# Kernel optimization log

Hardware: AMD Instinct MI355X
Metric: run time of the kernel (lower is better)

Reference implementation:

```python
import jax, jax.numpy as jnp
import numpy as np

TOP_K = 8


def setup_inputs() -> dict:
    key = jax.random.key(0)
    ks = jax.random.split(key, 8)
    B, S, H, BD, N, VBD = 4, 2048, 2048, 256, 256, 256
    return {
        "hidden_states": jax.random.normal(ks[0], (B, S, H), jnp.float32),
        "primary_attention_output": jax.random.normal(ks[1], (B, S, H), jnp.float32),
        "q_proj_w": jax.random.normal(ks[2], (BD, H), jnp.float32) / np.sqrt(H),
        "slot_keys": jax.random.normal(ks[3], (N, BD), jnp.float32),
        "slot_values": jax.random.normal(ks[4], (N, H), jnp.float32),
        "reliability": jax.random.uniform(ks[5], (N,), jnp.float32, 1e-3, 1.0),
        "value_down_w": jax.random.normal(ks[6], (VBD, H), jnp.float32) * 0.1 / np.sqrt(H),
        "value_up_w": jax.random.normal(ks[7], (H, VBD), jnp.float32) * 0.1 / np.sqrt(VBD),
    }


def reference(hidden_states, primary_attention_output, q_proj_w, slot_keys,
              slot_values, reliability, value_down_w, value_up_w):
    B, S, H = hidden_states.shape
    BD = q_proj_w.shape[0]
    # query = q_proj(hidden_states): [B,S,BD]
    query = jnp.einsum("bsh,dh->bsd", hidden_states, q_proj_w)
    # gate-chain scoring: query . slot_keys scaled, plus log-reliability mask
    rel_mask = jnp.log(jnp.clip(reliability, 1e-10))            # [N]
    scores = jnp.einsum("bsd,nd->bsn", query, slot_keys) / jnp.sqrt(
        jnp.asarray(BD, query.dtype)) + rel_mask                # [B,S,N]
    top_scores, top_idx = jax.lax.top_k(scores, TOP_K)          # [B,S,K]
    attn = jax.nn.softmax(top_scores, axis=-1)                  # [B,S,K]
    final_gate = jax.nn.sigmoid(top_scores[..., 0])             # [B,S]
    # slot-pool gather + weighted sum of values (irregular access)
    vals = slot_values[top_idx]                                 # [B,S,K,H]
    aux = jnp.einsum("bsk,bskh->bsh", attn, vals)               # [B,S,H]
    # low-rank value projection with GELU
    aux = jnp.einsum("bsh,vh->bsv", aux, value_down_w)
    aux = jax.nn.gelu(aux)
    aux = jnp.einsum("bsv,hv->bsh", aux, value_up_w)
    return primary_attention_output + final_gate[..., None] * aux
```

## Files before the change

### kernel.cpp

```cpp
#include <hip/hip_runtime.h>
#include <stdint.h>


typedef float f32x4 __attribute__((ext_vector_type(4)));
typedef unsigned short u16x8 __attribute__((ext_vector_type(8)));
typedef unsigned short u16x4 __attribute__((ext_vector_type(4)));
typedef __bf16 bf16x8 __attribute__((ext_vector_type(8)));

#define WS_QW    0u
#define WS_SK    1048576u
#define WS_SV    1179648u
#define WS_VDW   2228224u
#define WS_VUP   3276800u
#define WS_REL   4325376u
#define WS_PV    4326400u
#define WS_GATE  4588544u
#define WS_QP    4621312u
#define WS_D     21398528u

static __device__ __forceinline__ unsigned short f2bf(float f) {
  union { float f; unsigned int u; } v; v.f = f;
  unsigned int r = v.u + 0x7FFFu + ((v.u >> 16) & 1u);
  return (unsigned short)(r >> 16);
}
static __device__ __forceinline__ bf16x8 as_bf16(u16x8 v) {
  return __builtin_bit_cast(bf16x8, v);
}
static __device__ __forceinline__ float gelu_tanh(float x) {
  float u = 0.7978845608028654f * (x + 0.044715f * x * x * x);
  return 0.5f * x * (1.0f + tanhf(u));
}

__global__ void k_prep(const float* __restrict__ qw, const float* __restrict__ sk,
                       const float* __restrict__ sv, const float* __restrict__ vdw,
                       const float* __restrict__ vup, const float* __restrict__ rel,
                       unsigned char* __restrict__ ws) {
  unsigned short* o_qw  = (unsigned short*)(ws + WS_QW);
  unsigned short* o_sk  = (unsigned short*)(ws + WS_SK);
  unsigned short* o_sv  = (unsigned short*)(ws + WS_SV);
  unsigned short* o_vdw = (unsigned short*)(ws + WS_VDW);
  unsigned short* o_vup = (unsigned short*)(ws + WS_VUP);
  float* o_rel = (float*)(ws + WS_REL);
  int tid = blockIdx.x * blockDim.x + threadIdx.x;
  int stride = gridDim.x * blockDim.x;
  for (int g = tid; g < 540736; g += stride) {
    const float* src; unsigned short* dst; int i;
    if      (g < 131072) { src = qw;  dst = o_qw;  i = g; }
    else if (g < 147456) { src = sk;  dst = o_sk;  i = g - 131072; }
    else if (g < 278528) { src = sv;  dst = o_sv;  i = g - 147456; }
    else if (g < 409600) { src = vdw; dst = o_vdw; i = g - 278528; }
    else if (g < 540672) { src = vup; dst = o_vup; i = g - 409600; }
    else {
      int i4 = (g - 540672) * 4;
      #pragma unroll
      for (int j = 0; j < 4; j++) o_rel[i4 + j] = logf(fmaxf(rel[i4 + j], 1e-10f));
      continue;
    }
    f32x4 v = *(const f32x4*)(src + (size_t)i * 4);
    u16x4 o;
    #pragma unroll
    for (int j = 0; j < 4; j++) o[j] = f2bf(v[j]);
    *(u16x4*)(dst + (size_t)i * 4) = o;
  }
}

__global__ __launch_bounds__(256, 2) void k_pv(unsigned char* __restrict__ ws) {
  const unsigned short* sv  = (const unsigned short*)(ws + WS_SV);
  const unsigned short* vdw = (const unsigned short*)(ws + WS_VDW);
  float* PV = (float*)(ws + WS_PV);
  __shared__ __align__(16) unsigned short As[32 * 64];
  __shared__ __align__(16) unsigned short Bs[32 * 64];
  int t = threadIdx.x, lane = t & 63, w = t >> 6;
  int nt = blockIdx.x >> 3, vt = blockIdx.x & 7;
  int mf = w >> 1, nf = w & 1;
  f32x4 acc = {0.f, 0.f, 0.f, 0.f};
  int r = t >> 3, c = t & 7;
  int sw8 = (c ^ (r & 7)) * 8;
  for (int k0 = 0; k0 < 2048; k0 += 64) {
    __syncthreads();
    *(u16x8*)&As[r * 64 + sw8] = *(const u16x8*)&sv[(size_t)(nt * 32 + r) * 2048 + k0 + c * 8];
    *(u16x8*)&Bs[r * 64 + sw8] = *(const u16x8*)&vdw[(size_t)(vt * 32 + r) * 2048 + k0 + c * 8];
    __syncthreads();
    #pragma unroll
    for (int kk = 0; kk < 2; kk++) {
      int ck = kk * 4 + (lane >> 4);
      int ar = mf * 16 + (lane & 15);
      int br = nf * 16 + (lane & 15);
      bf16x8 a = as_bf16(*(const u16x8*)&As[ar * 64 + ((ck ^ (ar & 7)) * 8)]);
      bf16x8 b = as_bf16(*(const u16x8*)&Bs[br * 64 + ((ck ^ (br & 7)) * 8)]);
      acc = __builtin_amdgcn_mfma_f32_16x16x32_bf16(a, b, acc, 0, 0, 0);
    }
  }
  int row = nt * 32 + mf * 16 + (lane >> 4) * 4;
  int col = vt * 32 + nf * 16 + (lane & 15);
  #pragma unroll
  for (int j = 0; j < 4; j++) PV[(row + j) * 256 + col] = acc[j];
}

__global__ __launch_bounds__(256, 4) void k_query(const float* __restrict__ hs,
                                                  unsigned char* __restrict__ ws) {
  const unsigned short* qw = (const unsigned short*)(ws + WS_QW);
  float* qp = (float*)(ws + WS_QP);
  __shared__ __align__(16) unsigned short As[32 * 64];
  __shared__ __align__(16) unsigned short Bs[256 * 64];
  int t = threadIdx.x, lane = t & 63, w = t >> 6;
  int rt = blockIdx.x >> 1, ks = blockIdx.x & 1;
  int row0 = rt * 32, kbase = ks * 1024;
  f32x4 acc[2][4] = {};
  int sr = t >> 3, sc = t & 7;
  const float* aptr = hs + (size_t)(row0 + sr) * 2048 + kbase + sc * 8;
  const unsigned short* bptr = qw + (size_t)sr * 2048 + kbase + sc * 8;
  f32x4 pa0, pa1;
  u16x8 pb0, pb1, pb2, pb3, pb4, pb5, pb6, pb7;
  pa0 = *(const f32x4*)(aptr);
  pa1 = *(const f32x4*)(aptr + 4);
  pb0 = *(const u16x8*)(bptr + (size_t)0 * 32 * 2048);
  pb1 = *(const u16x8*)(bptr + (size_t)1 * 32 * 2048);
  pb2 = *(const u16x8*)(bptr + (size_t)2 * 32 * 2048);
  pb3 = *(const u16x8*)(bptr + (size_t)3 * 32 * 2048);
  pb4 = *(const u16x8*)(bptr + (size_t)4 * 32 * 2048);
  pb5 = *(const u16x8*)(bptr + (size_t)5 * 32 * 2048);
  pb6 = *(const u16x8*)(bptr + (size_t)6 * 32 * 2048);
  pb7 = *(const u16x8*)(bptr + (size_t)7 * 32 * 2048);
  for (int kt = 0; kt < 16; kt++) {
    __syncthreads();
    {
      u16x8 o;
      #pragma unroll
      for (int j = 0; j < 4; j++) { o[j] = f2bf(pa0[j]); o[4 + j] = f2bf(pa1[j]); }
      *(u16x8*)&As[sr * 64 + ((sc ^ (sr & 7)) * 8)] = o;
      u16x8 pb[8] = {pb0, pb1, pb2, pb3, pb4, pb5, pb6, pb7};
      #pragma unroll
      for (int i = 0; i < 8; i++) {
        int n = i * 32 + sr;
        *(u16x8*)&Bs[n * 64 + ((sc ^ (n & 7)) * 8)] = pb[i];
      }
    }
    __syncthreads();
    if (kt < 15) {
      int off = (kt + 1) * 64;
      pa0 = *(const f32x4*)(aptr + off);
      pa1 = *(const f32x4*)(aptr + off + 4);
      pb0 = *(const u16x8*)(bptr + (size_t)0 * 32 * 2048 + off);
      pb1 = *(const u16x8*)(bptr + (size_t)1 * 32 * 2048 + off);
      pb2 = *(const u16x8*)(bptr + (size_t)2 * 32 * 2048 + off);
      pb3 = *(const u16x8*)(bptr + (size_t)3 * 32 * 2048 + off);
      pb4 = *(const u16x8*)(bptr + (size_t)4 * 32 * 2048 + off);
      pb5 = *(const u16x8*)(bptr + (size_t)5 * 32 * 2048 + off);
      pb6 = *(const u16x8*)(bptr + (size_t)6 * 32 * 2048 + off);
      pb7 = *(const u16x8*)(bptr + (size_t)7 * 32 * 2048 + off);
    }
    #pragma unroll
    for (int kk = 0; kk < 2; kk++) {
      int ck = kk * 4 + (lane >> 4);
      bf16x8 a[2], b[4];
      #pragma unroll
      for (int mf = 0; mf < 2; mf++) {
        int arow = mf * 16 + (lane & 15);
        a[mf] = as_bf16(*(const u16x8*)&As[arow * 64 + ((ck ^ (arow & 7)) * 8)]);
      }
      #pragma unroll
      for (int nf = 0; nf < 4; nf++) {
        int brow = w * 64 + nf * 16 + (lane & 15);
        b[nf] = as_bf16(*(const u16x8*)&Bs[brow * 64 + ((ck ^ (brow & 7)) * 8)]);
      }
      #pragma unroll
      for (int mf = 0; mf < 2; mf++)
        #pragma unroll
        for (int nf = 0; nf < 4; nf++)
          acc[mf][nf] = __builtin_amdgcn_mfma_f32_16x16x32_bf16(a[mf], b[nf], acc[mf][nf], 0, 0, 0);
    }
  }
  float* outp = qp + (size_t)ks * 8192 * 256;
  #pragma unroll
  for (int mf = 0; mf < 2; mf++) {
    int row = row0 + mf * 16 + (lane >> 4) * 4;
    #pragma unroll
    for (int nf = 0; nf < 4; nf++) {
      int col = w * 64 + nf * 16 + (lane & 15);
      #pragma unroll
      for (int j = 0; j < 4; j++) outp[(size_t)(row + j) * 256 + col] = acc[mf][nf][j];
    }
  }
}

#define QSTR 264
#define SSTR 260
__global__ __launch_bounds__(256, 4) void k_score(unsigned char* __restrict__ ws) {
  const float* qp = (const float*)(ws + WS_QP);
  const unsigned short* sk = (const unsigned short*)(ws + WS_SK);
  const float* relm = (const float*)(ws + WS_REL);
  const float* PV = (const float*)(ws + WS_PV);
  float* gates = (float*)(ws + WS_GATE);
  unsigned short* D = (unsigned short*)(ws + WS_D);
  __shared__ __align__(16) unsigned short Qs[16 * QSTR];
  __shared__ __align__(16) float Ss[16 * SSTR];
  int t = threadIdx.x, lane = t & 63, w = t >> 6;
  int row0 = blockIdx.x * 16;
  #pragma unroll
  for (int i = 0; i < 4; i++) {
    int id = i * 256 + t, r = id >> 6, c4 = id & 63;
    const float* p0 = qp + (size_t)(row0 + r) * 256 + c4 * 4;
    f32x4 a = *(const f32x4*)p0;
    f32x4 b = *(const f32x4*)(p0 + 8192 * 256);
    u16x4 o;
    #pragma unroll
    for (int j = 0; j < 4; j++) o[j] = f2bf(a[j] + b[j]);
    *(u16x4*)&Qs[r * QSTR + c4 * 4] = o;
  }
  __syncthreads();
  {
    f32x4 acc[4] = {};
    for (int ksb = 0; ksb < 8; ksb++) {
      int ck = lane >> 4;
      bf16x8 a = as_bf16(*(const u16x8*)&Qs[(lane & 15) * QSTR + ksb * 32 + ck * 8]);
      #pragma unroll
      for (int nf = 0; nf < 4; nf++) {
        int n = w * 64 + nf * 16 + (lane & 15);
        bf16x8 b = as_bf16(*(const u16x8*)&sk[(size_t)n * 256 + ksb * 32 + ck * 8]);
        acc[nf] = __builtin_amdgcn_mfma_f32_16x16x32_bf16(a, b, acc[nf], 0, 0, 0);
      }
    }
    #pragma unroll
    for (int nf = 0; nf < 4; nf++) {
      int n = w * 64 + nf * 16 + (lane & 15);
      float rm = relm[n];
      int rr = (lane >> 4) * 4;
      #pragma unroll
      for (int j = 0; j < 4; j++) Ss[(rr + j) * SSTR + n] = acc[nf][j] * 0.0625f + rm;
    }
  }
  __syncthreads();
  for (int rr = 0; rr < 4; rr++) {
    int row = w * 4 + rr;
    f32x4 sv4 = *(const f32x4*)&Ss[row * SSTR + lane * 4];
    unsigned int key[4];
    #pragma unroll
    for (int j = 0; j < 4; j++) {
      unsigned int u = __builtin_bit_cast(unsigned int, sv4[j]);
      unsigned int os = (u & 0x80000000u) ? ~u : (u | 0x80000000u);
      key[j] = (os & 0xFFFFFF00u) | (unsigned int)(255 - (lane * 4 + j));
    }
    unsigned int win[8];
    #pragma unroll
    for (int e = 0; e < 8; e++) {
      unsigned int m01 = key[0] > key[1] ? key[0] : key[1];
      unsigned int m23 = key[2] > key[3] ? key[2] : key[3];
      unsigned int m = m01 > m23 ? m01 : m23;
      #pragma unroll
      for (int d = 1; d < 64; d <<= 1) {
        unsigned int o = (unsigned int)__shfl_xor((int)m, d, 64);
        m = o > m ? o : m;
      }
      win[e] = m;
      #pragma unroll
      for (int j = 0; j < 4; j++) if (key[j] == m) key[j] = 0u;
    }
    float s8[8]; int i8[8];
    #pragma unroll
    for (int e = 0; e < 8; e++) {
      i8[e] = 255 - (int)(win[e] & 0xFFu);
      unsigned int os = win[e] & 0xFFFFFF00u;
      unsigned int u = (os & 0x80000000u) ? (os ^ 0x80000000u) : ~os;
      s8[e] = __builtin_bit_cast(float, u);
    }
    float m0 = s8[0], sum = 0.f, we[8];
    #pragma unroll
    for (int e = 0; e < 8; e++) { we[e] = expf(s8[e] - m0); sum += we[e]; }
    float inv = 1.f / sum;
    f32x4 accv = {0.f, 0.f, 0.f, 0.f};
    #pragma unroll
    for (int e = 0; e < 8; e++) {
      float wk = we[e] * inv;
      f32x4 p = *(const f32x4*)(PV + (size_t)i8[e] * 256 + lane * 4);
      #pragma unroll
      for (int j = 0; j < 4; j++) accv[j] += wk * p[j];
    }
    u16x4 o;
    #pragma unroll
    for (int j = 0; j < 4; j++) o[j] = f2bf(gelu_tanh(accv[j]));
    *(u16x4*)&D[(size_t)(row0 + row) * 256 + lane * 4] = o;
    if (lane == 0) gates[row0 + row] = 1.f / (1.f + expf(-m0));
  }
}

union KOutLds {
  unsigned short AB[12288];
  float stage[32 * 132];
};
__global__ __launch_bounds__(256, 4) void k_out(const float* __restrict__ primary,
                                                float* __restrict__ out,
                                                unsigned char* __restrict__ ws) {
  const unsigned short* D = (const unsigned short*)(ws + WS_D);
  const unsigned short* vup = (const unsigned short*)(ws + WS_VUP);
  const float* gates = (const float*)(ws + WS_GATE);
  __shared__ __align__(16) KOutLds u;
  __shared__ float gate_s[64];
  unsigned short* As = u.AB;
  unsigned short* Bs = u.AB + 4096;
  int t = threadIdx.x, lane = t & 63, w = t >> 6;
  int bid = blockIdx.x;
  int L = (bid & 7) * 256 + (bid >> 3);
  int rt = L >> 4, ct = L & 15;
  int wm = w >> 1, wn = w & 1;
  const float* pbase = primary + (size_t)(rt * 64 + (t >> 5)) * 2048 + ct * 128 + (t & 31) * 4;
  f32x4 pref[2][4];
  #pragma unroll
  for (int i = 0; i < 4; i++)
    pref[0][i] = *(const f32x4*)(pbase + (size_t)(i * 8) * 2048);
  int sr = t >> 3, sc = t & 7;
  const unsigned short* aptr = D + (size_t)(rt * 64 + sr) * 256 + sc * 8;
  const unsigned short* bptr = vup + (size_t)(ct * 128 + sr) * 256 + sc * 8;
  u16x8 pA0, pA1, pB0, pB1, pB2, pB3;
  pA0 = *(const u16x8*)(aptr);
  pA1 = *(const u16x8*)(aptr + 32 * 256);
  pB0 = *(const u16x8*)(bptr);
  pB1 = *(const u16x8*)(bptr + 32 * 256);
  pB2 = *(const u16x8*)(bptr + 64 * 256);
  pB3 = *(const u16x8*)(bptr + 96 * 256);
  if (t < 64) gate_s[t] = gates[rt * 64 + t];
  f32x4 acc[2][4] = {};
  for (int k0 = 0; k0 < 256; k0 += 64) {
    __syncthreads();
    {
      int r0 = sr, r1 = sr + 32, r2 = sr + 64, r3 = sr + 96;
      *(u16x8*)&As[r0 * 64 + ((sc ^ (r0 & 7)) * 8)] = pA0;
      *(u16x8*)&As[r1 * 64 + ((sc ^ (r1 & 7)) * 8)] = pA1;
      *(u16x8*)&Bs[r0 * 64 + ((sc ^ (r0 & 7)) * 8)] = pB0;
      *(u16x8*)&Bs[r1 * 64 + ((sc ^ (r1 & 7)) * 8)] = pB1;
      *(u16x8*)&Bs[r2 * 64 + ((sc ^ (r2 & 7)) * 8)] = pB2;
      *(u16x8*)&Bs[r3 * 64 + ((sc ^ (r3 & 7)) * 8)] = pB3;
    }
    __syncthreads();
    if (k0 < 192) {
      int off = k0 + 64;
      pA0 = *(const u16x8*)(aptr + off);
      pA1 = *(const u16x8*)(aptr + 32 * 256 + off);
      pB0 = *(const u16x8*)(bptr + off);
      pB1 = *(const u16x8*)(bptr + 32 * 256 + off);
      pB2 = *(const u16x8*)(bptr + 64 * 256 + off);
      pB3 = *(const u16x8*)(bptr + 96 * 256 + off);
    }
    #pragma unroll
    for (int kk = 0; kk < 2; kk++) {
      int ck = kk * 4 + (lane >> 4);
      bf16x8 a[2], b[4];
      #pragma unroll
      for (int mf = 0; mf < 2; mf++) {
        int ar = wm * 32 + mf * 16 + (lane & 15);
        a[mf] = as_bf16(*(const u16x8*)&As[ar * 64 + ((ck ^ (ar & 7)) * 8)]);
      }
      #pragma unroll
      for (int nf = 0; nf < 4; nf++) {
        int br = wn * 64 + nf * 16 + (lane & 15);
        b[nf] = as_bf16(*(const u16x8*)&Bs[br * 64 + ((ck ^ (br & 7)) * 8)]);
      }
      #pragma unroll
      for (int mf = 0; mf < 2; mf++)
        #pragma unroll
        for (int nf = 0; nf < 4; nf++)
          acc[mf][nf] = __builtin_amdgcn_mfma_f32_16x16x32_bf16(a[mf], b[nf], acc[mf][nf], 0, 0, 0);
    }
  }
  #pragma unroll
  for (int c = 0; c < 2; c++) {
    __syncthreads();
    if (wm == c) {
      #pragma unroll
      for (int mf = 0; mf < 2; mf++) {
        #pragma unroll
        for (int nf = 0; nf < 4; nf++) {
          int col = wn * 64 + nf * 16 + (lane & 15);
          #pragma unroll
          for (int j = 0; j < 4; j++) {
            int r = mf * 16 + (lane >> 4) * 4 + j;
            u.stage[r * 132 + col] = acc[mf][nf][j];
          }
        }
      }
    }
    if (c == 0) {
      #pragma unroll
      for (int i = 0; i < 4; i++)
        pref[1][i] = *(const f32x4*)(pbase + (size_t)(32 + i * 8) * 2048);
    }
    __syncthreads();
    #pragma unroll
    for (int i = 0; i < 4; i++) {
      int idx = i * 256 + t, r = idx >> 5, c4 = idx & 31;
      int row = rt * 64 + c * 32 + r;
      size_t o = (size_t)row * 2048 + ct * 128 + c4 * 4;
      f32x4 p = pref[c][i];
      f32x4 s = *(const f32x4*)&u.stage[r * 132 + c4 * 4];
      float g = gate_s[c * 32 + r];
      f32x4 ov;
      #pragma unroll
      for (int j = 0; j < 4; j++) ov[j] = p[j] + g * s[j];
      *(f32x4*)(out + o) = ov;
    }
  }
}

extern "C" void kernel_launch(void* const* d_in, const int* in_sizes, int n_in,
                              void* d_out, int out_size, void* d_ws, size_t ws_size,
                              hipStream_t stream) {
  const float* hs      = (const float*)d_in[0];
  const float* primary = (const float*)d_in[1];
  const float* qw      = (const float*)d_in[2];
  const float* sk      = (const float*)d_in[3];
  const float* sv      = (const float*)d_in[4];
  const float* rel     = (const float*)d_in[5];
  const float* vdw     = (const float*)d_in[6];
  const float* vup     = (const float*)d_in[7];
  unsigned char* ws = (unsigned char*)d_ws;
  float* out = (float*)d_out;

  k_prep<<<dim3(256), dim3(256), 0, stream>>>(qw, sk, sv, vdw, vup, rel, ws);
  k_pv<<<dim3(64), dim3(256), 0, stream>>>(ws);
  k_query<<<dim3(512), dim3(256), 0, stream>>>(hs, ws);
  k_score<<<dim3(512), dim3(256), 0, stream>>>(ws);
  k_out<<<dim3(2048), dim3(256), 0, stream>>>(primary, out, ws);
}
```

Baseline: 94.36 us.

## Fuse query projection into scoring kernel and raise k_out occupancy bound

Result: slower. 137.1 us (+45.3%).

```diff
diff --git a/kernel.cpp b/kernel.cpp
--- a/kernel.cpp
+++ b/kernel.cpp
@@ -15,7 +15,6 @@
 #define WS_REL   4325376u
 #define WS_PV    4326400u
 #define WS_GATE  4588544u
-#define WS_QP    4621312u
 #define WS_D     21398528u
 
 static __device__ __forceinline__ unsigned short f2bf(float f) {
@@ -97,23 +96,34 @@
   for (int j = 0; j < 4; j++) PV[(row + j) * 256 + col] = acc[j];
 }
 
-__global__ __launch_bounds__(256, 4) void k_query(const float* __restrict__ hs,
-                                                  unsigned char* __restrict__ ws) {
+#define QSTR 264
+#define SSTR 260
+union QScoreLds {
+  unsigned short B[256 * 64];
+  struct {
+    unsigned short Qs[16 * QSTR];
+    float Ss[16 * SSTR];
+  } s;
+};
+__global__ __launch_bounds__(256, 4) void k_qscore(const float* __restrict__ hs,
+                                                   unsigned char* __restrict__ ws) {
   const unsigned short* qw = (const unsigned short*)(ws + WS_QW);
-  float* qp = (float*)(ws + WS_QP);
-  __shared__ __align__(16) unsigned short As[32 * 64];
-  __shared__ __align__(16) unsigned short Bs[256 * 64];
+  const unsigned short* sk = (const unsigned short*)(ws + WS_SK);
+  const float* relm = (const float*)(ws + WS_REL);
+  const float* PV = (const float*)(ws + WS_PV);
+  float* gates = (float*)(ws + WS_GATE);
+  unsigned short* D = (unsigned short*)(ws + WS_D);
+  __shared__ __align__(16) unsigned short As[16 * 64];
+  __shared__ __align__(16) QScoreLds u;
   int t = threadIdx.x, lane = t & 63, w = t >> 6;
-  int rt = blockIdx.x >> 1, ks = blockIdx.x & 1;
-  int row0 = rt * 32, kbase = ks * 1024;
-  f32x4 acc[2][4] = {};
+  int row0 = blockIdx.x * 16;
   int sr = t >> 3, sc = t & 7;
-  const float* aptr = hs + (size_t)(row0 + sr) * 2048 + kbase + sc * 8;
-  const unsigned short* bptr = qw + (size_t)sr * 2048 + kbase + sc * 8;
+  int asr = (t & 127) >> 3;
+  const float* aptr = hs + (size_t)(row0 + asr) * 2048 + sc * 8;
+  const unsigned short* bptr = qw + (size_t)sr * 2048 + sc * 8;
   f32x4 pa0, pa1;
   u16x8 pb0, pb1, pb2, pb3, pb4, pb5, pb6, pb7;
-  pa0 = *(const f32x4*)(aptr);
-  pa1 = *(const f32x4*)(aptr + 4);
+  if (t < 128) { pa0 = *(const f32x4*)(aptr); pa1 = *(const f32x4*)(aptr + 4); }
   pb0 = *(const u16x8*)(bptr + (size_t)0 * 32 * 2048);
   pb1 = *(const u16x8*)(bptr + (size_t)1 * 32 * 2048);
   pb2 = *(const u16x8*)(bptr + (size_t)2 * 32 * 2048);
@@ -122,25 +132,27 @@
   pb5 = *(const u16x8*)(bptr + (size_t)5 * 32 * 2048);
   pb6 = *(const u16x8*)(bptr + (size_t)6 * 32 * 2048);
   pb7 = *(const u16x8*)(bptr + (size_t)7 * 32 * 2048);
-  for (int kt = 0; kt < 16; kt++) {
-    __syncthreads();
+  f32x4 accq[4] = {};
+  for (int kt = 0; kt < 32; kt++) {
+    __syncthreads();
+    if (t < 128) {
+      u16x8 o;
+      #pragma unroll
+      for (int j = 0; j < 4; j++) { o[j] = f2bf(pa0[j]); o[4 + j] = f2bf(pa1[j]); }
+      *(u16x8*)&As[asr * 64 + ((sc ^ (asr & 7)) * 8)] = o;
+    }
     {
-      u16x8 o;
-      #pragma unroll
-      for (int j = 0; j < 4; j++) { o[j] = f2bf(pa0[j]); o[4 + j] = f2bf(pa1[j]); }
-      *(u16x8*)&As[sr * 64 + ((sc ^ (sr & 7)) * 8)] = o;
       u16x8 pb[8] = {pb0, pb1, pb2, pb3, pb4, pb5, pb6, pb7};
       #pragma unroll
       for (int i = 0; i < 8; i++) {
         int n = i * 32 + sr;
-        *(u16x8*)&Bs[n * 64 + ((sc ^ (n & 7)) * 8)] = pb[i];
-      }
-    }
-    __syncthreads();
-    if (kt < 15) {
+        *(u16x8*)&u.B[n * 64 + ((sc ^ (n & 7)) * 8)] = pb[i];
+      }
+    }
+    __syncthreads();
+    if (kt < 31) {
       int off = (kt + 1) * 64;
-      pa0 = *(const f32x4*)(aptr + off);
-      pa1 = *(const f32x4*)(aptr + off + 4);
+      if (t < 128) { pa0 = *(const f32x4*)(aptr + off); pa1 = *(const f32x4*)(aptr + off + 4); }
       pb0 = *(const u16x8*)(bptr + (size_t)0 * 32 * 2048 + off);
       pb1 = *(const u16x8*)(bptr + (size_t)1 * 32 * 2048 + off);
       pb2 = *(const u16x8*)(bptr + (size_t)2 * 32 * 2048 + off);
@@ -153,67 +165,31 @@
     #pragma unroll
     for (int kk = 0; kk < 2; kk++) {
       int ck = kk * 4 + (lane >> 4);
-      bf16x8 a[2], b[4];
-      #pragma unroll
-      for (int mf = 0; mf < 2; mf++) {
-        int arow = mf * 16 + (lane & 15);
-        a[mf] = as_bf16(*(const u16x8*)&As[arow * 64 + ((ck ^ (arow & 7)) * 8)]);
-      }
+      int arow = lane & 15;
+      bf16x8 a = as_bf16(*(const u16x8*)&As[arow * 64 + ((ck ^ (arow & 7)) * 8)]);
       #pragma unroll
       for (int nf = 0; nf < 4; nf++) {
         int brow = w * 64 + nf * 16 + (lane & 15);
-        b[nf] = as_bf16(*(const u16x8*)&Bs[brow * 64 + ((ck ^ (brow & 7)) * 8)]);
-      }
-      #pragma unroll
-      for (int mf = 0; mf < 2; mf++)
-        #pragma unroll
-        for (int nf = 0; nf < 4; nf++)
-          acc[mf][nf] = __builtin_amdgcn_mfma_f32_16x16x32_bf16(a[mf], b[nf], acc[mf][nf], 0, 0, 0);
-    }
-  }
-  float* outp = qp + (size_t)ks * 8192 * 256;
+        bf16x8 b = as_bf16(*(const u16x8*)&u.B[brow * 64 + ((ck ^ (brow & 7)) * 8)]);
+        accq[nf] = __builtin_amdgcn_mfma_f32_16x16x32_bf16(a, b, accq[nf], 0, 0, 0);
+      }
+    }
+  }
+  __syncthreads();
   #pragma unroll
-  for (int mf = 0; mf < 2; mf++) {
-    int row = row0 + mf * 16 + (lane >> 4) * 4;
-    #pragma unroll
-    for (int nf = 0; nf < 4; nf++) {
-      int col = w * 64 + nf * 16 + (lane & 15);
-      #pragma unroll
-      for (int j = 0; j < 4; j++) outp[(size_t)(row + j) * 256 + col] = acc[mf][nf][j];
-    }
-  }
-}
-
-#define QSTR 264
-#define SSTR 260
-__global__ __launch_bounds__(256, 4) void k_score(unsigned char* __restrict__ ws) {
-  const float* qp = (const float*)(ws + WS_QP);
-  const unsigned short* sk = (const unsigned short*)(ws + WS_SK);
-  const float* relm = (const float*)(ws + WS_REL);
-  const float* PV = (const float*)(ws + WS_PV);
-  float* gates = (float*)(ws + WS_GATE);
-  unsigned short* D = (unsigned short*)(ws + WS_D);
-  __shared__ __align__(16) unsigned short Qs[16 * QSTR];
-  __shared__ __align__(16) float Ss[16 * SSTR];
-  int t = threadIdx.x, lane = t & 63, w = t >> 6;
-  int row0 = blockIdx.x * 16;
-  #pragma unroll
-  for (int i = 0; i < 4; i++) {
-    int id = i * 256 + t, r = id >> 6, c4 = id & 63;
-    const float* p0 = qp + (size_t)(row0 + r) * 256 + c4 * 4;
-    f32x4 a = *(const f32x4*)p0;
-    f32x4 b = *(const f32x4*)(p0 + 8192 * 256);
-    u16x4 o;
-    #pragma unroll
-    for (int j = 0; j < 4; j++) o[j] = f2bf(a[j] + b[j]);
-    *(u16x4*)&Qs[r * QSTR + c4 * 4] = o;
+  for (int nf = 0; nf < 4; nf++) {
+    int col = w * 64 + nf * 16 + (lane & 15);
+    int rr = (lane >> 4) * 4;
+    #pragma unroll
+    for (int j = 0; j < 4; j++)
+      u.s.Qs[(rr + j) * QSTR + col] = f2bf(accq[nf][j]);
   }
   __syncthreads();
   {
     f32x4 acc[4] = {};
     for (int ksb = 0; ksb < 8; ksb++) {
       int ck = lane >> 4;
-      bf16x8 a = as_bf16(*(const u16x8*)&Qs[(lane & 15) * QSTR + ksb * 32 + ck * 8]);
+      bf16x8 a = as_bf16(*(const u16x8*)&u.s.Qs[(lane & 15) * QSTR + ksb * 32 + ck * 8]);
       #pragma unroll
       for (int nf = 0; nf < 4; nf++) {
         int n = w * 64 + nf * 16 + (lane & 15);
@@ -227,18 +203,18 @@
       float rm = relm[n];
       int rr = (lane >> 4) * 4;
       #pragma unroll
-      for (int j = 0; j < 4; j++) Ss[(rr + j) * SSTR + n] = acc[nf][j] * 0.0625f + rm;
+      for (int j = 0; j < 4; j++) u.s.Ss[(rr + j) * SSTR + n] = acc[nf][j] * 0.0625f + rm;
     }
   }
   __syncthreads();
   for (int rr = 0; rr < 4; rr++) {
     int row = w * 4 + rr;
-    f32x4 sv4 = *(const f32x4*)&Ss[row * SSTR + lane * 4];
+    f32x4 sv4 = *(const f32x4*)&u.s.Ss[row * SSTR + lane * 4];
     unsigned int key[4];
     #pragma unroll
     for (int j = 0; j < 4; j++) {
-      unsigned int u = __builtin_bit_cast(unsigned int, sv4[j]);
-      unsigned int os = (u & 0x80000000u) ? ~u : (u | 0x80000000u);
+      unsigned int uu = __builtin_bit_cast(unsigned int, sv4[j]);
+      unsigned int os = (uu & 0x80000000u) ? ~uu : (uu | 0x80000000u);
       key[j] = (os & 0xFFFFFF00u) | (unsigned int)(255 - (lane * 4 + j));
     }
     unsigned int win[8];
@@ -261,8 +237,8 @@
     for (int e = 0; e < 8; e++) {
       i8[e] = 255 - (int)(win[e] & 0xFFu);
       unsigned int os = win[e] & 0xFFFFFF00u;
-      unsigned int u = (os & 0x80000000u) ? (os ^ 0x80000000u) : ~os;
-      s8[e] = __builtin_bit_cast(float, u);
+      unsigned int uu = (os & 0x80000000u) ? (os ^ 0x80000000u) : ~os;
+      s8[e] = __builtin_bit_cast(float, uu);
     }
     float m0 = s8[0], sum = 0.f, we[8];
     #pragma unroll
@@ -288,7 +264,7 @@
   unsigned short AB[12288];
   float stage[32 * 132];
 };
-__global__ __launch_bounds__(256, 4) void k_out(const float* __restrict__ primary,
+__global__ __launch_bounds__(256, 6) void k_out(const float* __restrict__ primary,
                                                 float* __restrict__ out,
                                                 unsigned char* __restrict__ ws) {
   const unsigned short* D = (const unsigned short*)(ws + WS_D);
@@ -417,7 +393,6 @@
 
   k_prep<<<dim3(256), dim3(256), 0, stream>>>(qw, sk, sv, vdw, vup, rel, ws);
   k_pv<<<dim3(64), dim3(256), 0, stream>>>(ws);
-  k_query<<<dim3(512), dim3(256), 0, stream>>>(hs, ws);
-  k_score<<<dim3(512), dim3(256), 0, stream>>>(ws);
+  k_qscore<<<dim3(512), dim3(256), 0, stream>>>(hs, ws);
   k_out<<<dim3(2048), dim3(256), 0, stream>>>(primary, out, ws);
 }
```

## Split PV GEMM K across waves with direct global loads and LDS reduction

Applied to the files above, without the earlier changes.

After: 83.79 us. 1.13x faster.

```diff
diff --git a/kernel.cpp b/kernel.cpp
--- a/kernel.cpp
+++ b/kernel.cpp
@@ -64,37 +64,34 @@
   }
 }
 
-__global__ __launch_bounds__(256, 2) void k_pv(unsigned char* __restrict__ ws) {
+__global__ __launch_bounds__(256, 4) void k_pv(unsigned char* __restrict__ ws) {
   const unsigned short* sv  = (const unsigned short*)(ws + WS_SV);
   const unsigned short* vdw = (const unsigned short*)(ws + WS_VDW);
   float* PV = (float*)(ws + WS_PV);
-  __shared__ __align__(16) unsigned short As[32 * 64];
-  __shared__ __align__(16) unsigned short Bs[32 * 64];
+  __shared__ float red[4][16][16];
   int t = threadIdx.x, lane = t & 63, w = t >> 6;
-  int nt = blockIdx.x >> 3, vt = blockIdx.x & 7;
-  int mf = w >> 1, nf = w & 1;
+  int nt = blockIdx.x >> 4, vt = blockIdx.x & 15;
+  const unsigned short* aLane = sv  + (size_t)(nt * 16 + (lane & 15)) * 2048 + (lane >> 4) * 8 + w * 512;
+  const unsigned short* bLane = vdw + (size_t)(vt * 16 + (lane & 15)) * 2048 + (lane >> 4) * 8 + w * 512;
   f32x4 acc = {0.f, 0.f, 0.f, 0.f};
-  int r = t >> 3, c = t & 7;
-  int sw8 = (c ^ (r & 7)) * 8;
-  for (int k0 = 0; k0 < 2048; k0 += 64) {
-    __syncthreads();
-    *(u16x8*)&As[r * 64 + sw8] = *(const u16x8*)&sv[(size_t)(nt * 32 + r) * 2048 + k0 + c * 8];
-    *(u16x8*)&Bs[r * 64 + sw8] = *(const u16x8*)&vdw[(size_t)(vt * 32 + r) * 2048 + k0 + c * 8];
-    __syncthreads();
-    #pragma unroll
-    for (int kk = 0; kk < 2; kk++) {
-      int ck = kk * 4 + (lane >> 4);
-      int ar = mf * 16 + (lane & 15);
-      int br = nf * 16 + (lane & 15);
-      bf16x8 a = as_bf16(*(const u16x8*)&As[ar * 64 + ((ck ^ (ar & 7)) * 8)]);
-      bf16x8 b = as_bf16(*(const u16x8*)&Bs[br * 64 + ((ck ^ (br & 7)) * 8)]);
-      acc = __builtin_amdgcn_mfma_f32_16x16x32_bf16(a, b, acc, 0, 0, 0);
-    }
-  }
-  int row = nt * 32 + mf * 16 + (lane >> 4) * 4;
-  int col = vt * 32 + nf * 16 + (lane & 15);
-  #pragma unroll
-  for (int j = 0; j < 4; j++) PV[(row + j) * 256 + col] = acc[j];
+  #pragma unroll
+  for (int kt = 0; kt < 16; kt++) {
+    bf16x8 a = as_bf16(*(const u16x8*)(aLane + kt * 32));
+    bf16x8 b = as_bf16(*(const u16x8*)(bLane + kt * 32));
+    acc = __builtin_amdgcn_mfma_f32_16x16x32_bf16(a, b, acc, 0, 0, 0);
+  }
+  int col = lane & 15, row0 = (lane >> 4) * 4;
+  #pragma unroll
+  for (int j = 0; j < 4; j++) red[w][row0 + j][col] = acc[j];
+  __syncthreads();
+  if (w == 0) {
+    #pragma unroll
+    for (int i = 0; i < 4; i++) {
+      int idx = i * 64 + lane, r = idx >> 4, c = idx & 15;
+      float s = red[0][r][c] + red[1][r][c] + red[2][r][c] + red[3][r][c];
+      PV[(nt * 16 + r) * 256 + vt * 16 + c] = s;
+    }
+  }
 }
 
 __global__ __launch_bounds__(256, 4) void k_query(const float* __restrict__ hs,
@@ -416,7 +413,7 @@
   float* out = (float*)d_out;
 
   k_prep<<<dim3(256), dim3(256), 0, stream>>>(qw, sk, sv, vdw, vup, rel, ws);
-  k_pv<<<dim3(64), dim3(256), 0, stream>>>(ws);
+  k_pv<<<dim3(256), dim3(256), 0, stream>>>(ws);
   k_query<<<dim3(512), dim3(256), 0, stream>>>(hs, ws);
   k_score<<<dim3(512), dim3(256), 0, stream>>>(ws);
   k_out<<<dim3(2048), dim3(256), 0, stream>>>(primary, out, ws);
```
